# Kernel optimization log

Measured on AMD Instinct MI355X. Metric: run time of the kernel, lower is better.

## Reference

```python
import jax, jax.numpy as jnp
import numpy as np

N_EMBED = 1024
N_HEAD = 16
BLOCK_SIZE = 2048
ROPE_BASE = 10000.0


def _rope_cache():
    # theta uses n_embed (full model dim) as denominator, as in the source,
    # then is truncated to head_size//2 frequencies.
    hs_half = N_EMBED // N_HEAD // 2
    j = jnp.arange(N_EMBED // 2, dtype=jnp.float32)
    theta = jnp.power(ROPE_BASE, -2.0 * j / N_EMBED)
    seq_idx = jnp.arange(BLOCK_SIZE, dtype=jnp.float32)
    idx_theta = jnp.einsum('i,j->ij', seq_idx, theta)[:, :hs_half]  # [block, hs/2]
    return jnp.stack([jnp.cos(idx_theta), jnp.sin(idx_theta)], axis=-1)  # [block, hs/2, 2]


def _apply_rope(x, cache):
    # x: [B, nh, T, hs]. FAITHFUL to source: rope indexes its cache by dim-1,
    # which here is the HEAD dim (rope is called after transpose(1,2)).
    B, d1, d2, hs = x.shape
    rc = cache[:d1, :hs // 2]            # [d1, hs/2, 2]
    rc = rc[None, :, None, :, :]          # [1, d1, 1, hs/2, 2]
    x2 = x.reshape(B, d1, d2, hs // 2, 2)
    cos, sin = rc[..., 0], rc[..., 1]
    xr, xi = x2[..., 0], x2[..., 1]
    rot = jnp.stack([xr * cos - xi * sin, xi * cos + xr * sin], axis=-1)
    return rot.reshape(B, d1, d2, hs).astype(x.dtype)


def setup_inputs() -> dict:
    key = jax.random.key(0)
    ks = jax.random.split(key, 5)
    B, T, C = 2, 2048, N_EMBED
    return {
        'x': jax.random.normal(ks[0], (B, T, C), dtype=jnp.float32),
        'w_attn': jax.random.normal(ks[1], (C, 3 * C), dtype=jnp.float32) * 0.02,
        'b_attn': jax.random.normal(ks[2], (3 * C,), dtype=jnp.float32) * 0.02,
        'w_proj': jax.random.normal(ks[3], (C, C), dtype=jnp.float32) * 0.02,
        'b_proj': jax.random.normal(ks[4], (C,), dtype=jnp.float32) * 0.02,
    }


def reference(x, w_attn, b_attn, w_proj, b_proj):
    B, T, C = x.shape
    nh, hs = N_HEAD, C // N_HEAD
    qkv = x @ w_attn + b_attn                     # [B, T, 3C]
    q, k, v = jnp.split(qkv, 3, axis=-1)
    q = q.reshape(B, T, nh, hs).transpose(0, 2, 1, 3)  # [B, nh, T, hs]
    k = k.reshape(B, T, nh, hs).transpose(0, 2, 1, 3)
    v = v.reshape(B, T, nh, hs).transpose(0, 2, 1, 3)
    cache = _rope_cache()
    q = _apply_rope(q, cache)
    k = _apply_rope(k, cache)
    scale = 1.0 / jnp.sqrt(jnp.asarray(hs, dtype=q.dtype))
    scores = jnp.einsum('bhqd,bhkd->bhqk', q, k) * scale
    causal = jnp.tril(jnp.ones((T, T), dtype=bool))
    scores = jnp.where(causal[None, None], scores, jnp.finfo(scores.dtype).min)
    attn = jax.nn.softmax(scores, axis=-1)
    y = jnp.einsum('bhqk,bhkd->bhqd', attn, v)    # [B, nh, T, hs]
    y = y.transpose(0, 2, 1, 3).reshape(B, T, C)
    return y @ w_proj + b_proj
```

## Files before the change

### kernel.cpp

```cpp
#include <hip/hip_runtime.h>
#include <hip/hip_bf16.h>
#include <math.h>

#define TSEQ 2048
#define CEMB 1024
#define NHEAD 16
#define HS 64

typedef __attribute__((ext_vector_type(8))) short bf16x8;
typedef __attribute__((ext_vector_type(4))) float f32x4;
typedef __attribute__((ext_vector_type(16))) float f32x16;
typedef unsigned int u32;
typedef unsigned long long u64;

__device__ __forceinline__ void gload16(const void* g, void* l) {
    __builtin_amdgcn_global_load_lds(
        (const __attribute__((address_space(1))) unsigned int*)g,
        (__attribute__((address_space(3))) unsigned int*)l, 16, 0, 0);
}

__device__ __forceinline__ u32 pk2(float a, float b) {
    union { u32 u; __hip_bfloat16 h[2]; } t;
    t.h[0] = __float2bfloat16(a); t.h[1] = __float2bfloat16(b);
    return t.u;
}

__global__ void rope_tbl_k(float* __restrict__ tbl) {
    int i = blockIdx.x * blockDim.x + threadIdx.x;
    if (i >= NHEAD * 32) return;
    int h = i >> 5, j = i & 31;
    double theta = pow(10000.0, -2.0 * (double)j / 1024.0);
    double ang = (double)h * theta;
    tbl[2 * i + 0] = (float)cos(ang);
    tbl[2 * i + 1] = (float)sin(ang);
}

__global__ __launch_bounds__(256) void cvt_bf16_k(const float* __restrict__ in,
                                                  __hip_bfloat16* __restrict__ out) {
    int i = (blockIdx.x * 256 + threadIdx.x) * 8;
    float4 a = *(const float4*)(in + i);
    float4 b = *(const float4*)(in + i + 4);
    union { bf16x8 v; __hip_bfloat16 h[8]; } pk;
    pk.h[0] = __float2bfloat16(a.x); pk.h[1] = __float2bfloat16(a.y);
    pk.h[2] = __float2bfloat16(a.z); pk.h[3] = __float2bfloat16(a.w);
    pk.h[4] = __float2bfloat16(b.x); pk.h[5] = __float2bfloat16(b.y);
    pk.h[6] = __float2bfloat16(b.z); pk.h[7] = __float2bfloat16(b.w);
    *(bf16x8*)(out + i) = pk.v;
}

__global__ __launch_bounds__(256) void transpose_bf16_k(const float* __restrict__ src,
                                                        __hip_bfloat16* __restrict__ dst,
                                                        int K, int N) {
    __shared__ float tile[32][33];
    int n0 = blockIdx.x * 32, k0 = blockIdx.y * 32;
    int tx = threadIdx.x & 31, ty = threadIdx.x >> 5;
#pragma unroll
    for (int i = 0; i < 32; i += 8)
        tile[ty + i][tx] = src[(size_t)(k0 + ty + i) * N + n0 + tx];
    __syncthreads();
#pragma unroll
    for (int i = 0; i < 32; i += 8)
        dst[(size_t)(n0 + ty + i) * K + k0 + tx] = __float2bfloat16(tile[tx][ty + i]);
}

__global__ __launch_bounds__(256) void qkv_mfma_k(
    const __hip_bfloat16* __restrict__ Xb, const __hip_bfloat16* __restrict__ Wt,
    const float* __restrict__ bias, const float* __restrict__ tbl,
    __hip_bfloat16* __restrict__ Qb, __hip_bfloat16* __restrict__ Kb,
    __hip_bfloat16* __restrict__ Vtb)
{
    __shared__ __hip_bfloat16 SM[4][128 * 32];
    const int tid = threadIdx.x;
    const int lane = tid & 63, w = tid >> 6;
    const int lr = lane & 15, lg = lane >> 4;
    const int wm = w >> 1, wn = w & 1;
    const int n0 = blockIdx.x * 128;
    const int m0 = blockIdx.y * 128;
    const __hip_bfloat16* gA = Xb + (size_t)(m0 + (tid >> 2)) * CEMB + (tid & 3) * 8;
    const __hip_bfloat16* gB = Wt + (size_t)(n0 + (tid >> 2)) * CEMB + (tid & 3) * 8;
#define QSTAGE(buf, kk) do { \
        gload16(gA + (kk), &SM[buf][tid * 8]); \
        gload16(gA + 64 * CEMB + (kk), &SM[buf][2048 + tid * 8]); \
        gload16(gB + (kk), &SM[2 + (buf)][tid * 8]); \
        gload16(gB + 64 * CEMB + (kk), &SM[2 + (buf)][2048 + tid * 8]); } while (0)
    f32x4 acc[4][4] = {};
    QSTAGE(0, 0);
    __syncthreads();
    for (int k0 = 0; k0 < CEMB; k0 += 32) {
        const int cur = (k0 >> 5) & 1;
        if (k0 + 32 < CEMB) QSTAGE(cur ^ 1, k0 + 32);
        bf16x8 af[4], bfr[4];
#pragma unroll
        for (int mi = 0; mi < 4; ++mi)
            af[mi] = *(const bf16x8*)&SM[cur][(wm * 64 + mi * 16 + lr) * 32 + lg * 8];
#pragma unroll
        for (int ni = 0; ni < 4; ++ni)
            bfr[ni] = *(const bf16x8*)&SM[2 + cur][(wn * 64 + ni * 16 + lr) * 32 + lg * 8];
#pragma unroll
        for (int mi = 0; mi < 4; ++mi)
#pragma unroll
            for (int ni = 0; ni < 4; ++ni)
                acc[mi][ni] = __builtin_amdgcn_mfma_f32_16x16x32_bf16(af[mi], bfr[ni], acc[mi][ni], 0, 0, 0);
        __syncthreads();
    }
    const int sec = (n0 >> 10);
    const int bb = m0 >> 11;
    const int t0v = m0 & 2047;
    if (sec == 2) {
        char* T = (char*)SM;
#pragma unroll
        for (int mi = 0; mi < 4; ++mi) {
#pragma unroll
            for (int ni = 0; ni < 4; ++ni) {
                const int nl = wn * 64 + ni * 16 + lr;
                const float bv = bias[n0 + nl];
                const int mb = wm * 64 + mi * 16 + lg * 4;
                union { u64 u; __hip_bfloat16 hh[4]; } pk;
#pragma unroll
                for (int r = 0; r < 4; ++r) pk.hh[r] = __float2bfloat16(acc[mi][ni][r] + bv);
                *(u64*)(T + nl * 256 + ((mb * 2) ^ ((nl & 7) << 4))) = pk.u;
            }
        }
        __syncthreads();
        const int h0 = (n0 & 1023) >> 6;
#pragma unroll
        for (int i = 0; i < 8; ++i) {
            int cid = tid + 256 * i;
            int n = cid >> 4, mc = cid & 15;
            bf16x8 v = *(const bf16x8*)(T + n * 256 + ((mc * 16) ^ ((n & 7) << 4)));
            *(bf16x8*)&Vtb[(((size_t)bb * NHEAD + h0 + (n >> 6)) * HS + (n & 63)) * TSEQ + t0v + mc * 8] = v;
        }
    } else {
#pragma unroll
        for (int mi = 0; mi < 4; ++mi) {
#pragma unroll
            for (int ni = 0; ni < 4; ++ni) {
                const int gcol = n0 + wn * 64 + ni * 16 + lr;
                const int c63 = gcol & 63;
                const int h = (gcol & 1023) >> 6;
                const int j = c63 >> 1;
                const float cth = tbl[(h * 32 + j) * 2 + 0];
                const float sth = tbl[(h * 32 + j) * 2 + 1];
                const float bv = bias[gcol];
                const int growb = m0 + wm * 64 + mi * 16 + lg * 4;
                const int t0 = growb & 2047;
                const float sc = (sec == 0) ? 0.18033688011112042f : 1.0f;
                __hip_bfloat16* dst = (sec == 0) ? Qb : Kb;
#pragma unroll
                for (int r = 0; r < 4; ++r) {
                    float val = acc[mi][ni][r] + bv;
                    float prt = __shfl_xor(val, 1);
                    float rot = (lr & 1) ? (val * cth + prt * sth) : (val * cth - prt * sth);
                    dst[(((size_t)bb * NHEAD + h) * TSEQ + t0 + r) * HS + c63] = __float2bfloat16(rot * sc);
                }
            }
        }
    }
#undef QSTAGE
}

__global__ __launch_bounds__(128) void attn_k(
    const __hip_bfloat16* __restrict__ Q, const __hip_bfloat16* __restrict__ K,
    const __hip_bfloat16* __restrict__ Vt, __hip_bfloat16* __restrict__ Y)
{
    __shared__ __hip_bfloat16 KsBuf[2][64 * 64];
    __shared__ __hip_bfloat16 VsBuf[2][64 * 64];
    const int tid = threadIdx.x;
    const int w = tid >> 6;
    const int lane = tid & 63;
    const int l31 = lane & 31;
    const int hi = lane >> 5;
    const int id = blockIdx.x;
    const int bh = id & 31;
    const int g = id >> 5, ga = g & 7, gb = g >> 3;
    const int qb = gb * 8 + ((gb & 1) ? (7 - ga) : ga);
    const size_t bho = (size_t)bh * TSEQ * HS;
    const int qw = qb * 64 + w * 32;

    int srcK[4], srcV[4];
#pragma unroll
    for (int j = 0; j < 4; ++j) {
        int L = (tid + 128 * j) * 16;
        int row = L >> 7;
        int ce = ((L & 127) ^ (((row ^ (row >> 3)) & 7) << 4)) >> 1;
        srcK[j] = row * HS + ce;
        srcV[j] = row * TSEQ + ce;
    }
    const __hip_bfloat16* Kg = K + bho;
    const __hip_bfloat16* Vg = Vt + bho;
#define ASTAGE(buf, kt_) do { \
        const __hip_bfloat16* kg_ = Kg + (size_t)(kt_) * 64 * HS; \
        const __hip_bfloat16* vg_ = Vg + (size_t)(kt_) * 64; \
        char* kb_ = (char*)KsBuf[buf]; char* vb_ = (char*)VsBuf[buf]; \
        _Pragma("unroll") \
        for (int j = 0; j < 4; ++j) { \
            gload16(kg_ + srcK[j], kb_ + (tid + 128 * j) * 16); \
            gload16(vg_ + srcV[j], vb_ + (tid + 128 * j) * 16); } } while (0)

    bf16x8 qf[4];
    {
        const __hip_bfloat16* qp = Q + bho + (size_t)(qw + l31) * HS + hi * 8;
#pragma unroll
        for (int kb = 0; kb < 4; ++kb) qf[kb] = *(const bf16x8*)(qp + kb * 16);
    }
    const int base0 = l31 * 128;
    const int swz0 = ((l31 ^ (l31 >> 3)) & 7) << 4;
    const int r32 = 32 + l31;
    const int base1 = r32 * 128;
    const int swz1 = ((r32 ^ (r32 >> 3)) & 7) << 4;

    float mrow = -1e30f, lsum = 0.f;
    f32x16 o0 = {}, o1 = {};

    ASTAGE(0, 0);
    __syncthreads();
    for (int kt = 0; kt <= qb; ++kt) {
        const int cur = kt & 1;
        if (kt < qb) ASTAGE(cur ^ 1, kt + 1);
        const char* KsB = (const char*)KsBuf[cur];
        const char* VsB = (const char*)VsBuf[cur];
        const bool do1 = (w == 1) || (kt < qb);
        f32x16 s0 = {}, s1 = {};
        __builtin_amdgcn_s_setprio(1);
#pragma unroll
        for (int kb = 0; kb < 4; ++kb) {
            bf16x8 kf = *(const bf16x8*)(KsB + base0 + ((kb * 32 + hi * 16) ^ swz0));
            s0 = __builtin_amdgcn_mfma_f32_32x32x16_bf16(kf, qf[kb], s0, 0, 0, 0);
        }
        if (do1) {
#pragma unroll
            for (int kb = 0; kb < 4; ++kb) {
                bf16x8 kf = *(const bf16x8*)(KsB + base1 + ((kb * 32 + hi * 16) ^ swz1));
                s1 = __builtin_amdgcn_mfma_f32_32x32x16_bf16(kf, qf[kb], s1, 0, 0, 0);
            }
        }
        __builtin_amdgcn_s_setprio(0);
        if (kt == qb) {
            if (w == 0) {
#pragma unroll
                for (int r = 0; r < 16; ++r) {
                    int crow = (r & 3) + 8 * (r >> 2) + 4 * hi;
                    if (crow > l31) s0[r] = -1e30f;
                }
            } else {
#pragma unroll
                for (int r = 0; r < 16; ++r) {
                    int crow = (r & 3) + 8 * (r >> 2) + 4 * hi;
                    if (crow > l31) s1[r] = -1e30f;
                }
            }
        }
        float mx = s0[0];
#pragma unroll
        for (int r = 1; r < 16; ++r) mx = fmaxf(mx, s0[r]);
        if (do1) {
#pragma unroll
            for (int r = 0; r < 16; ++r) mx = fmaxf(mx, s1[r]);
        }
        mx = fmaxf(mx, __shfl_xor(mx, 32));
        const float mn = fmaxf(mrow, mx);
        const float alpha = __builtin_amdgcn_exp2f(mrow - mn);
        mrow = mn;
        float ls = 0.f;
#pragma unroll
        for (int r = 0; r < 16; ++r) { s0[r] = __builtin_amdgcn_exp2f(s0[r] - mn); ls += s0[r]; }
        if (do1) {
#pragma unroll
            for (int r = 0; r < 16; ++r) { s1[r] = __builtin_amdgcn_exp2f(s1[r] - mn); ls += s1[r]; }
        }
        ls += __shfl_xor(ls, 32);
        lsum = lsum * alpha + ls;
        o0 = o0 * alpha;
        o1 = o1 * alpha;
        union { u32 u[4]; bf16x8 v; } pa[4];
        {
            u32 w01 = pk2(s0[0], s0[1]),   w23 = pk2(s0[2], s0[3]);
            u32 w45 = pk2(s0[4], s0[5]),   w67 = pk2(s0[6], s0[7]);
            u32 w89 = pk2(s0[8], s0[9]),   wab = pk2(s0[10], s0[11]);
            u32 wcd = pk2(s0[12], s0[13]), wef = pk2(s0[14], s0[15]);
            u32 xa = __shfl_xor(hi ? w01 : w45, 32);
            u32 xb = __shfl_xor(hi ? w23 : w67, 32);
            u32 xc = __shfl_xor(hi ? w89 : wcd, 32);
            u32 xd = __shfl_xor(hi ? wab : wef, 32);
            if (hi == 0) {
                pa[0].u[0] = w01; pa[0].u[1] = w23; pa[0].u[2] = xa;  pa[0].u[3] = xb;
                pa[1].u[0] = w89; pa[1].u[1] = wab; pa[1].u[2] = xc;  pa[1].u[3] = xd;
            } else {
                pa[0].u[0] = xa;  pa[0].u[1] = xb;  pa[0].u[2] = w45; pa[0].u[3] = w67;
                pa[1].u[0] = xc;  pa[1].u[1] = xd;  pa[1].u[2] = wcd; pa[1].u[3] = wef;
            }
        }
        if (do1) {
            u32 w01 = pk2(s1[0], s1[1]),   w23 = pk2(s1[2], s1[3]);
            u32 w45 = pk2(s1[4], s1[5]),   w67 = pk2(s1[6], s1[7]);
            u32 w89 = pk2(s1[8], s1[9]),   wab = pk2(s1[10], s1[11]);
            u32 wcd = pk2(s1[12], s1[13]), wef = pk2(s1[14], s1[15]);
            u32 xa = __shfl_xor(hi ? w01 : w45, 32);
            u32 xb = __shfl_xor(hi ? w23 : w67, 32);
            u32 xc = __shfl_xor(hi ? w89 : wcd, 32);
            u32 xd = __shfl_xor(hi ? wab : wef, 32);
            if (hi == 0) {
                pa[2].u[0] = w01; pa[2].u[1] = w23; pa[2].u[2] = xa;  pa[2].u[3] = xb;
                pa[3].u[0] = w89; pa[3].u[1] = wab; pa[3].u[2] = xc;  pa[3].u[3] = xd;
            } else {
                pa[2].u[0] = xa;  pa[2].u[1] = xb;  pa[2].u[2] = w45; pa[2].u[3] = w67;
                pa[3].u[0] = xc;  pa[3].u[1] = xd;  pa[3].u[2] = wcd; pa[3].u[3] = wef;
            }
        }
        __builtin_amdgcn_s_setprio(1);
#pragma unroll
        for (int ks = 0; ks < 2; ++ks) {
            bf16x8 vf0 = *(const bf16x8*)(VsB + base0 + ((ks * 32 + hi * 16) ^ swz0));
            o0 = __builtin_amdgcn_mfma_f32_32x32x16_bf16(vf0, pa[ks].v, o0, 0, 0, 0);
            bf16x8 vf1 = *(const bf16x8*)(VsB + base1 + ((ks * 32 + hi * 16) ^ swz1));
            o1 = __builtin_amdgcn_mfma_f32_32x32x16_bf16(vf1, pa[ks].v, o1, 0, 0, 0);
        }
        if (do1) {
#pragma unroll
            for (int ks = 2; ks < 4; ++ks) {
                bf16x8 vf0 = *(const bf16x8*)(VsB + base0 + ((ks * 32 + hi * 16) ^ swz0));
                o0 = __builtin_amdgcn_mfma_f32_32x32x16_bf16(vf0, pa[ks].v, o0, 0, 0, 0);
                bf16x8 vf1 = *(const bf16x8*)(VsB + base1 + ((ks * 32 + hi * 16) ^ swz1));
                o1 = __builtin_amdgcn_mfma_f32_32x32x16_bf16(vf1, pa[ks].v, o1, 0, 0, 0);
            }
        }
        __builtin_amdgcn_s_setprio(0);
        __syncthreads();
    }
    __syncthreads();
    {
        char* T = (char*)KsBuf[0] + w * 4096;
        const float inv = 1.f / lsum;
        const int tsw = (l31 & 7) << 4;
#pragma unroll
        for (int r = 0; r < 16; ++r) {
            int d0 = (r & 3) + 8 * (r >> 2) + 4 * hi;
            *(__hip_bfloat16*)(T + base0 + ((d0 * 2) ^ tsw)) = __float2bfloat16(o0[r] * inv);
            *(__hip_bfloat16*)(T + base0 + (((d0 + 32) * 2) ^ tsw)) = __float2bfloat16(o1[r] * inv);
        }
        const int b = bh >> 4, h = bh & 15;
#pragma unroll
        for (int p = 0; p < 4; ++p) {
            int q = p * 8 + (lane >> 3);
            int colb = ((lane & 7) * 16) ^ ((q & 7) << 4);
            bf16x8 v = *(const bf16x8*)(T + q * 128 + colb);
            *(bf16x8*)(Y + ((size_t)b * TSEQ + qw + q) * CEMB + h * HS + (lane & 7) * 8) = v;
        }
    }
#undef ASTAGE
}

__global__ __launch_bounds__(256) void proj_mfma_k(
    const __hip_bfloat16* __restrict__ Ab, const __hip_bfloat16* __restrict__ Wt,
    const float* __restrict__ bias, float* __restrict__ out)
{
    __shared__ __hip_bfloat16 Al[2][128 * 32];
    __shared__ __hip_bfloat16 Bl[2][128 * 32];
    const int tid = threadIdx.x;
    const int lane = tid & 63, w = tid >> 6;
    const int lr = lane & 15, lg = lane >> 4;
    const int wm = w >> 1, wn = w & 1;
    const int n0 = blockIdx.x * 128;
    const int m0 = blockIdx.y * 128;
    const __hip_bfloat16* gA = Ab + (size_t)(m0 + (tid >> 2)) * CEMB + (tid & 3) * 8;
    const __hip_bfloat16* gB = Wt + (size_t)(n0 + (tid >> 2)) * CEMB + (tid & 3) * 8;
#define PSTAGE(buf, kk) do { \
        gload16(gA + (kk), &Al[buf][tid * 8]); \
        gload16(gA + 64 * CEMB + (kk), &Al[buf][2048 + tid * 8]); \
        gload16(gB + (kk), &Bl[buf][tid * 8]); \
        gload16(gB + 64 * CEMB + (kk), &Bl[buf][2048 + tid * 8]); } while (0)
    f32x4 acc[4][4] = {};
    PSTAGE(0, 0);
    __syncthreads();
    for (int k0 = 0; k0 < CEMB; k0 += 32) {
        const int cur = (k0 >> 5) & 1;
        if (k0 + 32 < CEMB) PSTAGE(cur ^ 1, k0 + 32);
        bf16x8 af[4], bfr[4];
#pragma unroll
        for (int mi = 0; mi < 4; ++mi)
            af[mi] = *(const bf16x8*)&Al[cur][(wm * 64 + mi * 16 + lr) * 32 + lg * 8];
#pragma unroll
        for (int ni = 0; ni < 4; ++ni)
            bfr[ni] = *(const bf16x8*)&Bl[cur][(wn * 64 + ni * 16 + lr) * 32 + lg * 8];
#pragma unroll
        for (int mi = 0; mi < 4; ++mi)
#pragma unroll
            for (int ni = 0; ni < 4; ++ni)
                acc[mi][ni] = __builtin_amdgcn_mfma_f32_16x16x32_bf16(af[mi], bfr[ni], acc[mi][ni], 0, 0, 0);
        __syncthreads();
    }
#pragma unroll
    for (int mi = 0; mi < 4; ++mi) {
#pragma unroll
        for (int ni = 0; ni < 4; ++ni) {
            const int gcol = n0 + wn * 64 + ni * 16 + lr;
            const float bv = bias[gcol];
            const int growb = m0 + wm * 64 + mi * 16 + lg * 4;
#pragma unroll
            for (int r = 0; r < 4; ++r)
                out[(size_t)(growb + r) * CEMB + gcol] = acc[mi][ni][r] + bv;
        }
    }
#undef PSTAGE
}

extern "C" void kernel_launch(void* const* d_in, const int* in_sizes, int n_in,
                              void* d_out, int out_size, void* d_ws, size_t ws_size,
                              hipStream_t stream)
{
    const float* x      = (const float*)d_in[0];
    const float* w_attn = (const float*)d_in[1];
    const float* b_attn = (const float*)d_in[2];
    const float* w_proj = (const float*)d_in[3];
    const float* b_proj = (const float*)d_in[4];
    float* out = (float*)d_out;
    char* base = (char*)d_ws;

    const size_t MB = 1048576;
    float* tbl          = (float*)base;
    __hip_bfloat16* Xb  = (__hip_bfloat16*)(base + 4096);
    __hip_bfloat16* Wta = (__hip_bfloat16*)(base + 4096 + 8 * MB);
    __hip_bfloat16* Wpt = (__hip_bfloat16*)(base + 4096 + 14 * MB);
    __hip_bfloat16* Qb  = (__hip_bfloat16*)(base + 4096 + 16 * MB);
    __hip_bfloat16* Kb  = (__hip_bfloat16*)(base + 4096 + 24 * MB);
    __hip_bfloat16* Vtb = (__hip_bfloat16*)(base + 4096 + 32 * MB);
    __hip_bfloat16* Yb  = Xb;

    rope_tbl_k<<<1, 512, 0, stream>>>(tbl);
    cvt_bf16_k<<<2048, 256, 0, stream>>>(x, Xb);
    transpose_bf16_k<<<dim3(96, 32), 256, 0, stream>>>(w_attn, Wta, CEMB, 3 * CEMB);
    transpose_bf16_k<<<dim3(32, 32), 256, 0, stream>>>(w_proj, Wpt, CEMB, CEMB);
    qkv_mfma_k<<<dim3(24, 32), 256, 0, stream>>>(Xb, Wta, b_attn, tbl, Qb, Kb, Vtb);
    attn_k<<<1024, 128, 0, stream>>>(Qb, Kb, Vtb, Yb);
    proj_mfma_k<<<dim3(8, 32), 256, 0, stream>>>(Yb, Wpt, b_proj, out);
}
```

Baseline: 147.6 us.

## Process 128-key tiles per iteration with single-buffered K/V instead of double buffering

The attention loop now consumes 128 keys per iteration (four 32-row score blocks) instead of 64, halving the number of iterations, softmax rescales and barriers. K/V staging goes from a double-buffered prefetch overlapped with compute to a single buffer loaded after each iteration's barrier, with a new V swizzle for the 256-byte rows. This trades away load/compute overlap and adds register pressure (four score accumulators, eight P fragments) in exchange for fewer loop overheads and more MFMA work per sync.

```diff
diff --git a/kernel.cpp b/kernel.cpp
--- a/kernel.cpp
+++ b/kernel.cpp
@@ -163,8 +163,8 @@
     const __hip_bfloat16* __restrict__ Q, const __hip_bfloat16* __restrict__ K,
     const __hip_bfloat16* __restrict__ Vt, __hip_bfloat16* __restrict__ Y)
 {
-    __shared__ __hip_bfloat16 KsBuf[2][64 * 64];
-    __shared__ __hip_bfloat16 VsBuf[2][64 * 64];
+    __shared__ __hip_bfloat16 Ks[128 * 64];
+    __shared__ __hip_bfloat16 Vs[64 * 128];
     const int tid = threadIdx.x;
     const int w = tid >> 6;
     const int lane = tid & 63;
@@ -177,23 +177,23 @@
     const size_t bho = (size_t)bh * TSEQ * HS;
     const int qw = qb * 64 + w * 32;
 
-    int srcK[4], srcV[4];
-#pragma unroll
-    for (int j = 0; j < 4; ++j) {
+    int srcK[8], srcV[8];
+#pragma unroll
+    for (int j = 0; j < 8; ++j) {
         int L = (tid + 128 * j) * 16;
-        int row = L >> 7;
-        int ce = ((L & 127) ^ (((row ^ (row >> 3)) & 7) << 4)) >> 1;
-        srcK[j] = row * HS + ce;
-        srcV[j] = row * TSEQ + ce;
+        int rk = L >> 7;
+        srcK[j] = rk * HS + (((L & 127) ^ (((rk ^ (rk >> 3)) & 7) << 4)) >> 1);
+        int rv = L >> 8;
+        srcV[j] = rv * TSEQ + (((L & 255) ^ ((rv & 15) << 4)) >> 1);
     }
     const __hip_bfloat16* Kg = K + bho;
     const __hip_bfloat16* Vg = Vt + bho;
-#define ASTAGE(buf, kt_) do { \
-        const __hip_bfloat16* kg_ = Kg + (size_t)(kt_) * 64 * HS; \
-        const __hip_bfloat16* vg_ = Vg + (size_t)(kt_) * 64; \
-        char* kb_ = (char*)KsBuf[buf]; char* vb_ = (char*)VsBuf[buf]; \
+#define ASTAGE(r_) do { \
+        const __hip_bfloat16* kg_ = Kg + (size_t)(r_) * 128 * HS; \
+        const __hip_bfloat16* vg_ = Vg + (size_t)(r_) * 128; \
+        char* kb_ = (char*)Ks; char* vb_ = (char*)Vs; \
         _Pragma("unroll") \
-        for (int j = 0; j < 4; ++j) { \
+        for (int j = 0; j < 8; ++j) { \
             gload16(kg_ + srcK[j], kb_ + (tid + 128 * j) * 16); \
             gload16(vg_ + srcV[j], vb_ + (tid + 128 * j) * 16); } } while (0)
 
@@ -203,59 +203,100 @@
 #pragma unroll
         for (int kb = 0; kb < 4; ++kb) qf[kb] = *(const bf16x8*)(qp + kb * 16);
     }
-    const int base0 = l31 * 128;
-    const int swz0 = ((l31 ^ (l31 >> 3)) & 7) << 4;
-    const int r32 = 32 + l31;
-    const int base1 = r32 * 128;
-    const int swz1 = ((r32 ^ (r32 >> 3)) & 7) << 4;
+    int kbase[4], kswz[4];
+#pragma unroll
+    for (int st = 0; st < 4; ++st) {
+        int row = st * 32 + l31;
+        kbase[st] = row * 128;
+        kswz[st] = ((row ^ (row >> 3)) & 7) << 4;
+    }
+    const int vswz = (l31 & 15) << 4;
+    const int vbase0 = l31 * 256;
+    const int vbase1 = (32 + l31) * 256;
 
     float mrow = -1e30f, lsum = 0.f;
     f32x16 o0 = {}, o1 = {};
 
-    ASTAGE(0, 0);
+    const int nr = (qb >> 1) + 1;
+    const int diag = 2 * (qb & 1) + w;
+
+    ASTAGE(0);
     __syncthreads();
-    for (int kt = 0; kt <= qb; ++kt) {
-        const int cur = kt & 1;
-        if (kt < qb) ASTAGE(cur ^ 1, kt + 1);
-        const char* KsB = (const char*)KsBuf[cur];
-        const char* VsB = (const char*)VsBuf[cur];
-        const bool do1 = (w == 1) || (kt < qb);
-        f32x16 s0 = {}, s1 = {};
+    for (int r = 0; r < nr; ++r) {
+        const bool last = (r == nr - 1);
+        const bool a1 = !last || (diag >= 1);
+        const bool a2 = !last || (diag >= 2);
+        const bool a3 = !last || (diag >= 3);
+        f32x16 s0 = {}, s1 = {}, s2 = {}, s3 = {};
         __builtin_amdgcn_s_setprio(1);
 #pragma unroll
         for (int kb = 0; kb < 4; ++kb) {
-            bf16x8 kf = *(const bf16x8*)(KsB + base0 + ((kb * 32 + hi * 16) ^ swz0));
+            bf16x8 kf = *(const bf16x8*)((const char*)Ks + kbase[0] + ((kb * 32 + hi * 16) ^ kswz[0]));
             s0 = __builtin_amdgcn_mfma_f32_32x32x16_bf16(kf, qf[kb], s0, 0, 0, 0);
         }
-        if (do1) {
+        if (a1) {
 #pragma unroll
             for (int kb = 0; kb < 4; ++kb) {
-                bf16x8 kf = *(const bf16x8*)(KsB + base1 + ((kb * 32 + hi * 16) ^ swz1));
+                bf16x8 kf = *(const bf16x8*)((const char*)Ks + kbase[1] + ((kb * 32 + hi * 16) ^ kswz[1]));
                 s1 = __builtin_amdgcn_mfma_f32_32x32x16_bf16(kf, qf[kb], s1, 0, 0, 0);
             }
         }
+        if (a2) {
+#pragma unroll
+            for (int kb = 0; kb < 4; ++kb) {
+                bf16x8 kf = *(const bf16x8*)((const char*)Ks + kbase[2] + ((kb * 32 + hi * 16) ^ kswz[2]));
+                s2 = __builtin_amdgcn_mfma_f32_32x32x16_bf16(kf, qf[kb], s2, 0, 0, 0);
+            }
+        }
+        if (a3) {
+#pragma unroll
+            for (int kb = 0; kb < 4; ++kb) {
+                bf16x8 kf = *(const bf16x8*)((const char*)Ks + kbase[3] + ((kb * 32 + hi * 16) ^ kswz[3]));
+                s3 = __builtin_amdgcn_mfma_f32_32x32x16_bf16(kf, qf[kb], s3, 0, 0, 0);
+            }
+        }
         __builtin_amdgcn_s_setprio(0);
-        if (kt == qb) {
-            if (w == 0) {
-#pragma unroll
-                for (int r = 0; r < 16; ++r) {
-                    int crow = (r & 3) + 8 * (r >> 2) + 4 * hi;
-                    if (crow > l31) s0[r] = -1e30f;
+        if (last) {
+            if (diag == 0) {
+#pragma unroll
+                for (int rr = 0; rr < 16; ++rr) {
+                    int crow = (rr & 3) + 8 * (rr >> 2) + 4 * hi;
+                    if (crow > l31) s0[rr] = -1e30f;
+                }
+            } else if (diag == 1) {
+#pragma unroll
+                for (int rr = 0; rr < 16; ++rr) {
+                    int crow = (rr & 3) + 8 * (rr >> 2) + 4 * hi;
+                    if (crow > l31) s1[rr] = -1e30f;
+                }
+            } else if (diag == 2) {
+#pragma unroll
+                for (int rr = 0; rr < 16; ++rr) {
+                    int crow = (rr & 3) + 8 * (rr >> 2) + 4 * hi;
+                    if (crow > l31) s2[rr] = -1e30f;
                 }
             } else {
 #pragma unroll
-                for (int r = 0; r < 16; ++r) {
-                    int crow = (r & 3) + 8 * (r >> 2) + 4 * hi;
-                    if (crow > l31) s1[r] = -1e30f;
+                for (int rr = 0; rr < 16; ++rr) {
+                    int crow = (rr & 3) + 8 * (rr >> 2) + 4 * hi;
+                    if (crow > l31) s3[rr] = -1e30f;
                 }
             }
         }
         float mx = s0[0];
 #pragma unroll
-        for (int r = 1; r < 16; ++r) mx = fmaxf(mx, s0[r]);
-        if (do1) {
-#pragma unroll
-            for (int r = 0; r < 16; ++r) mx = fmaxf(mx, s1[r]);
+        for (int rr = 1; rr < 16; ++rr) mx = fmaxf(mx, s0[rr]);
+        if (a1) {
+#pragma unroll
+            for (int rr = 0; rr < 16; ++rr) mx = fmaxf(mx, s1[rr]);
+        }
+        if (a2) {
+#pragma unroll
+            for (int rr = 0; rr < 16; ++rr) mx = fmaxf(mx, s2[rr]);
+        }
+        if (a3) {
+#pragma unroll
+            for (int rr = 0; rr < 16; ++rr) mx = fmaxf(mx, s3[rr]);
         }
         mx = fmaxf(mx, __shfl_xor(mx, 32));
         const float mn = fmaxf(mrow, mx);
@@ -263,80 +304,73 @@
         mrow = mn;
         float ls = 0.f;
 #pragma unroll
-        for (int r = 0; r < 16; ++r) { s0[r] = __builtin_amdgcn_exp2f(s0[r] - mn); ls += s0[r]; }
-        if (do1) {
-#pragma unroll
-            for (int r = 0; r < 16; ++r) { s1[r] = __builtin_amdgcn_exp2f(s1[r] - mn); ls += s1[r]; }
+        for (int rr = 0; rr < 16; ++rr) { s0[rr] = __builtin_amdgcn_exp2f(s0[rr] - mn); ls += s0[rr]; }
+        if (a1) {
+#pragma unroll
+            for (int rr = 0; rr < 16; ++rr) { s1[rr] = __builtin_amdgcn_exp2f(s1[rr] - mn); ls += s1[rr]; }
+        }
+        if (a2) {
+#pragma unroll
+            for (int rr = 0; rr < 16; ++rr) { s2[rr] = __builtin_amdgcn_exp2f(s2[rr] - mn); ls += s2[rr]; }
+        }
+        if (a3) {
+#pragma unroll
+            for (int rr = 0; rr < 16; ++rr) { s3[rr] = __builtin_amdgcn_exp2f(s3[rr] - mn); ls += s3[rr]; }
         }
         ls += __shfl_xor(ls, 32);
         lsum = lsum * alpha + ls;
         o0 = o0 * alpha;
         o1 = o1 * alpha;
-        union { u32 u[4]; bf16x8 v; } pa[4];
-        {
-            u32 w01 = pk2(s0[0], s0[1]),   w23 = pk2(s0[2], s0[3]);
-            u32 w45 = pk2(s0[4], s0[5]),   w67 = pk2(s0[6], s0[7]);
-            u32 w89 = pk2(s0[8], s0[9]),   wab = pk2(s0[10], s0[11]);
-            u32 wcd = pk2(s0[12], s0[13]), wef = pk2(s0[14], s0[15]);
-            u32 xa = __shfl_xor(hi ? w01 : w45, 32);
-            u32 xb = __shfl_xor(hi ? w23 : w67, 32);
-            u32 xc = __shfl_xor(hi ? w89 : wcd, 32);
-            u32 xd = __shfl_xor(hi ? wab : wef, 32);
-            if (hi == 0) {
-                pa[0].u[0] = w01; pa[0].u[1] = w23; pa[0].u[2] = xa;  pa[0].u[3] = xb;
-                pa[1].u[0] = w89; pa[1].u[1] = wab; pa[1].u[2] = xc;  pa[1].u[3] = xd;
-            } else {
-                pa[0].u[0] = xa;  pa[0].u[1] = xb;  pa[0].u[2] = w45; pa[0].u[3] = w67;
-                pa[1].u[0] = xc;  pa[1].u[1] = xd;  pa[1].u[2] = wcd; pa[1].u[3] = wef;
-            }
-        }
-        if (do1) {
-            u32 w01 = pk2(s1[0], s1[1]),   w23 = pk2(s1[2], s1[3]);
-            u32 w45 = pk2(s1[4], s1[5]),   w67 = pk2(s1[6], s1[7]);
-            u32 w89 = pk2(s1[8], s1[9]),   wab = pk2(s1[10], s1[11]);
-            u32 wcd = pk2(s1[12], s1[13]), wef = pk2(s1[14], s1[15]);
-            u32 xa = __shfl_xor(hi ? w01 : w45, 32);
-            u32 xb = __shfl_xor(hi ? w23 : w67, 32);
-            u32 xc = __shfl_xor(hi ? w89 : wcd, 32);
-            u32 xd = __shfl_xor(hi ? wab : wef, 32);
-            if (hi == 0) {
-                pa[2].u[0] = w01; pa[2].u[1] = w23; pa[2].u[2] = xa;  pa[2].u[3] = xb;
-                pa[3].u[0] = w89; pa[3].u[1] = wab; pa[3].u[2] = xc;  pa[3].u[3] = xd;
-            } else {
-                pa[2].u[0] = xa;  pa[2].u[1] = xb;  pa[2].u[2] = w45; pa[2].u[3] = w67;
-                pa[3].u[0] = xc;  pa[3].u[1] = xd;  pa[3].u[2] = wcd; pa[3].u[3] = wef;
-            }
-        }
+        union { u32 u[4]; bf16x8 v; } pa[8];
+#define PACK(S, P0, P1) do { \
+            u32 w01 = pk2(S[0], S[1]),   w23 = pk2(S[2], S[3]); \
+            u32 w45 = pk2(S[4], S[5]),   w67 = pk2(S[6], S[7]); \
+            u32 w89 = pk2(S[8], S[9]),   wab = pk2(S[10], S[11]); \
+            u32 wcd = pk2(S[12], S[13]), wef = pk2(S[14], S[15]); \
+            u32 xa = __shfl_xor(hi ? w01 : w45, 32); \
+            u32 xb = __shfl_xor(hi ? w23 : w67, 32); \
+            u32 xc = __shfl_xor(hi ? w89 : wcd, 32); \
+            u32 xd = __shfl_xor(hi ? wab : wef, 32); \
+            if (hi == 0) { \
+                pa[P0].u[0] = w01; pa[P0].u[1] = w23; pa[P0].u[2] = xa;  pa[P0].u[3] = xb; \
+                pa[P1].u[0] = w89; pa[P1].u[1] = wab; pa[P1].u[2] = xc;  pa[P1].u[3] = xd; \
+            } else { \
+                pa[P0].u[0] = xa;  pa[P0].u[1] = xb;  pa[P0].u[2] = w45; pa[P0].u[3] = w67; \
+                pa[P1].u[0] = xc;  pa[P1].u[1] = xd;  pa[P1].u[2] = wcd; pa[P1].u[3] = wef; \
+            } } while (0)
+        PACK(s0, 0, 1);
+        if (a1) PACK(s1, 2, 3);
+        if (a2) PACK(s2, 4, 5);
+        if (a3) PACK(s3, 6, 7);
+#undef PACK
         __builtin_amdgcn_s_setprio(1);
-#pragma unroll
-        for (int ks = 0; ks < 2; ++ks) {
-            bf16x8 vf0 = *(const bf16x8*)(VsB + base0 + ((ks * 32 + hi * 16) ^ swz0));
-            o0 = __builtin_amdgcn_mfma_f32_32x32x16_bf16(vf0, pa[ks].v, o0, 0, 0, 0);
-            bf16x8 vf1 = *(const bf16x8*)(VsB + base1 + ((ks * 32 + hi * 16) ^ swz1));
-            o1 = __builtin_amdgcn_mfma_f32_32x32x16_bf16(vf1, pa[ks].v, o1, 0, 0, 0);
-        }
-        if (do1) {
-#pragma unroll
-            for (int ks = 2; ks < 4; ++ks) {
-                bf16x8 vf0 = *(const bf16x8*)(VsB + base0 + ((ks * 32 + hi * 16) ^ swz0));
-                o0 = __builtin_amdgcn_mfma_f32_32x32x16_bf16(vf0, pa[ks].v, o0, 0, 0, 0);
-                bf16x8 vf1 = *(const bf16x8*)(VsB + base1 + ((ks * 32 + hi * 16) ^ swz1));
-                o1 = __builtin_amdgcn_mfma_f32_32x32x16_bf16(vf1, pa[ks].v, o1, 0, 0, 0);
-            }
-        }
+#define PVC(ks) do { \
+            bf16x8 vf0 = *(const bf16x8*)((const char*)Vs + vbase0 + (((ks) * 32 + hi * 16) ^ vswz)); \
+            o0 = __builtin_amdgcn_mfma_f32_32x32x16_bf16(vf0, pa[ks].v, o0, 0, 0, 0); \
+            bf16x8 vf1 = *(const bf16x8*)((const char*)Vs + vbase1 + (((ks) * 32 + hi * 16) ^ vswz)); \
+            o1 = __builtin_amdgcn_mfma_f32_32x32x16_bf16(vf1, pa[ks].v, o1, 0, 0, 0); } while (0)
+        PVC(0); PVC(1);
+        if (a1) { PVC(2); PVC(3); }
+        if (a2) { PVC(4); PVC(5); }
+        if (a3) { PVC(6); PVC(7); }
+#undef PVC
         __builtin_amdgcn_s_setprio(0);
         __syncthreads();
-    }
-    __syncthreads();
+        if (r + 1 < nr) {
+            ASTAGE(r + 1);
+            __syncthreads();
+        }
+    }
     {
-        char* T = (char*)KsBuf[0] + w * 4096;
+        char* T = (char*)Ks + w * 4096;
         const float inv = 1.f / lsum;
         const int tsw = (l31 & 7) << 4;
-#pragma unroll
-        for (int r = 0; r < 16; ++r) {
-            int d0 = (r & 3) + 8 * (r >> 2) + 4 * hi;
-            *(__hip_bfloat16*)(T + base0 + ((d0 * 2) ^ tsw)) = __float2bfloat16(o0[r] * inv);
-            *(__hip_bfloat16*)(T + base0 + (((d0 + 32) * 2) ^ tsw)) = __float2bfloat16(o1[r] * inv);
+        const int tbase = l31 * 128;
+#pragma unroll
+        for (int rr = 0; rr < 16; ++rr) {
+            int d0 = (rr & 3) + 8 * (rr >> 2) + 4 * hi;
+            *(__hip_bfloat16*)(T + tbase + ((d0 * 2) ^ tsw)) = __float2bfloat16(o0[rr] * inv);
+            *(__hip_bfloat16*)(T + tbase + (((d0 + 32) * 2) ^ tsw)) = __float2bfloat16(o1[rr] * inv);
         }
         const int b = bh >> 4, h = bh & 15;
 #pragma unroll
```

After: 151.5 us. 1.03x slower.

## Split long causal attention rows across two blocks and merge partial softmax

Applied to the files above, without the earlier changes.

Replaces the 128-thread per-64-query attention kernel with a 256-thread kernel over 128-query tiles. The long tiles (query blocks 8-15) are split into two KV halves whose partial outputs, maxima and sums are written to workspace in fp32. A new merge kernel then combines them into bf16 Y, with a static unit table ordering blocks for load balance. The aim is to remove the tail imbalance of causal attention at the cost of an extra launch, fp32 partial traffic, and a fallback to the old kernel when the workspace is too small.

```diff
diff --git a/kernel.cpp b/kernel.cpp
--- a/kernel.cpp
+++ b/kernel.cpp
@@ -24,6 +24,10 @@
     t.h[0] = __float2bfloat16(a); t.h[1] = __float2bfloat16(b);
     return t.u;
 }
+
+__device__ const int UNIT_TBL[24] = {22,7,20,21,19,17,6,14,
+                                     23,18,16,12,4,5,13,15,
+                                     0,1,2,3,10,8,9,11};
 
 __global__ void rope_tbl_k(float* __restrict__ tbl) {
     int i = blockIdx.x * blockDim.x + threadIdx.x;
@@ -159,7 +163,245 @@
 #undef QSTAGE
 }
 
-__global__ __launch_bounds__(128) void attn_k(
+__global__ __launch_bounds__(256) void attn_split_k(
+    const __hip_bfloat16* __restrict__ Q, const __hip_bfloat16* __restrict__ K,
+    const __hip_bfloat16* __restrict__ Vt, __hip_bfloat16* __restrict__ Y,
+    float* __restrict__ Op, float* __restrict__ Mp, float* __restrict__ Lp)
+{
+    __shared__ __hip_bfloat16 KsBuf[2][64 * 64];
+    __shared__ __hip_bfloat16 VsBuf[2][64 * 64];
+    const int tid = threadIdx.x;
+    const int w = tid >> 6;
+    const int lane = tid & 63;
+    const int l31 = lane & 31;
+    const int hi = lane >> 5;
+    const int id = blockIdx.x;
+    const int bh = id & 31;
+    const int u = UNIT_TBL[id >> 5];
+    int qbb, kt0, ktN, half;
+    bool split;
+    if (u < 8) { qbb = u; half = 0; kt0 = 0; ktN = 2 * u + 2; split = false; }
+    else {
+        qbb = 8 + ((u - 8) >> 1); half = (u - 8) & 1;
+        kt0 = half ? (qbb + 1) : 0;
+        ktN = half ? (2 * qbb + 2) : (qbb + 1);
+        split = true;
+    }
+    const size_t bho = (size_t)bh * TSEQ * HS;
+    const int Qw = qbb * 128 + w * 32;
+
+    int srcK[2], srcV[2];
+#pragma unroll
+    for (int j = 0; j < 2; ++j) {
+        int L = (tid + 256 * j) * 16;
+        int row = L >> 7;
+        int ce = ((L & 127) ^ (((row ^ (row >> 3)) & 7) << 4)) >> 1;
+        srcK[j] = row * HS + ce;
+        srcV[j] = row * TSEQ + ce;
+    }
+    const __hip_bfloat16* Kg = K + bho;
+    const __hip_bfloat16* Vg = Vt + bho;
+#define ASTAGE(buf, kt_) do { \
+        const __hip_bfloat16* kg_ = Kg + (size_t)(kt_) * 64 * HS; \
+        const __hip_bfloat16* vg_ = Vg + (size_t)(kt_) * 64; \
+        char* kb_ = (char*)KsBuf[buf]; char* vb_ = (char*)VsBuf[buf]; \
+        _Pragma("unroll") \
+        for (int j = 0; j < 2; ++j) { \
+            gload16(kg_ + srcK[j], kb_ + (tid + 256 * j) * 16); \
+            gload16(vg_ + srcV[j], vb_ + (tid + 256 * j) * 16); } } while (0)
+
+    bf16x8 qf[4];
+    {
+        const __hip_bfloat16* qp = Q + bho + (size_t)(Qw + l31) * HS + hi * 8;
+#pragma unroll
+        for (int kb = 0; kb < 4; ++kb) qf[kb] = *(const bf16x8*)(qp + kb * 16);
+    }
+    const int base0 = l31 * 128;
+    const int swz0 = ((l31 ^ (l31 >> 3)) & 7) << 4;
+    const int r32 = 32 + l31;
+    const int base1 = r32 * 128;
+    const int swz1 = ((r32 ^ (r32 >> 3)) & 7) << 4;
+
+    float mrow = -1e30f, lsum = 0.f;
+    f32x16 o0 = {}, o1 = {};
+
+    ASTAGE(0, kt0);
+    __syncthreads();
+    for (int kt = kt0; kt < ktN; ++kt) {
+        const int cur = (kt - kt0) & 1;
+        if (kt + 1 < ktN) ASTAGE(cur ^ 1, kt + 1);
+        const char* KsB = (const char*)KsBuf[cur];
+        const char* VsB = (const char*)VsBuf[cur];
+        const int kvb0 = kt * 64, kvb1 = kt * 64 + 32;
+        const bool do0 = kvb0 <= Qw;
+        const bool do1 = kvb1 <= Qw;
+        if (do0) {
+            f32x16 s0 = {}, s1 = {};
+            __builtin_amdgcn_s_setprio(1);
+#pragma unroll
+            for (int kb = 0; kb < 4; ++kb) {
+                bf16x8 kf = *(const bf16x8*)(KsB + base0 + ((kb * 32 + hi * 16) ^ swz0));
+                s0 = __builtin_amdgcn_mfma_f32_32x32x16_bf16(kf, qf[kb], s0, 0, 0, 0);
+            }
+            if (do1) {
+#pragma unroll
+                for (int kb = 0; kb < 4; ++kb) {
+                    bf16x8 kf = *(const bf16x8*)(KsB + base1 + ((kb * 32 + hi * 16) ^ swz1));
+                    s1 = __builtin_amdgcn_mfma_f32_32x32x16_bf16(kf, qf[kb], s1, 0, 0, 0);
+                }
+            }
+            __builtin_amdgcn_s_setprio(0);
+            if (kvb0 == Qw) {
+#pragma unroll
+                for (int r = 0; r < 16; ++r) {
+                    int crow = (r & 3) + 8 * (r >> 2) + 4 * hi;
+                    if (crow > l31) s0[r] = -1e30f;
+                }
+            }
+            if (do1 && kvb1 == Qw) {
+#pragma unroll
+                for (int r = 0; r < 16; ++r) {
+                    int crow = (r & 3) + 8 * (r >> 2) + 4 * hi;
+                    if (crow > l31) s1[r] = -1e30f;
+                }
+            }
+            float mx = s0[0];
+#pragma unroll
+            for (int r = 1; r < 16; ++r) mx = fmaxf(mx, s0[r]);
+            if (do1) {
+#pragma unroll
+                for (int r = 0; r < 16; ++r) mx = fmaxf(mx, s1[r]);
+            }
+            mx = fmaxf(mx, __shfl_xor(mx, 32));
+            const float mn = fmaxf(mrow, mx);
+            const float alpha = __builtin_amdgcn_exp2f(mrow - mn);
+            mrow = mn;
+            float ls = 0.f;
+#pragma unroll
+            for (int r = 0; r < 16; ++r) { s0[r] = __builtin_amdgcn_exp2f(s0[r] - mn); ls += s0[r]; }
+            if (do1) {
+#pragma unroll
+                for (int r = 0; r < 16; ++r) { s1[r] = __builtin_amdgcn_exp2f(s1[r] - mn); ls += s1[r]; }
+            }
+            ls += __shfl_xor(ls, 32);
+            lsum = lsum * alpha + ls;
+            o0 = o0 * alpha;
+            o1 = o1 * alpha;
+            union { u32 u[4]; bf16x8 v; } pa[4];
+            {
+                u32 w01 = pk2(s0[0], s0[1]),   w23 = pk2(s0[2], s0[3]);
+                u32 w45 = pk2(s0[4], s0[5]),   w67 = pk2(s0[6], s0[7]);
+                u32 w89 = pk2(s0[8], s0[9]),   wab = pk2(s0[10], s0[11]);
+                u32 wcd = pk2(s0[12], s0[13]), wef = pk2(s0[14], s0[15]);
+                u32 xa = __shfl_xor(hi ? w01 : w45, 32);
+                u32 xb = __shfl_xor(hi ? w23 : w67, 32);
+                u32 xc = __shfl_xor(hi ? w89 : wcd, 32);
+                u32 xd = __shfl_xor(hi ? wab : wef, 32);
+                if (hi == 0) {
+                    pa[0].u[0] = w01; pa[0].u[1] = w23; pa[0].u[2] = xa;  pa[0].u[3] = xb;
+                    pa[1].u[0] = w89; pa[1].u[1] = wab; pa[1].u[2] = xc;  pa[1].u[3] = xd;
+                } else {
+                    pa[0].u[0] = xa;  pa[0].u[1] = xb;  pa[0].u[2] = w45; pa[0].u[3] = w67;
+                    pa[1].u[0] = xc;  pa[1].u[1] = xd;  pa[1].u[2] = wcd; pa[1].u[3] = wef;
+                }
+            }
+            if (do1) {
+                u32 w01 = pk2(s1[0], s1[1]),   w23 = pk2(s1[2], s1[3]);
+                u32 w45 = pk2(s1[4], s1[5]),   w67 = pk2(s1[6], s1[7]);
+                u32 w89 = pk2(s1[8], s1[9]),   wab = pk2(s1[10], s1[11]);
+                u32 wcd = pk2(s1[12], s1[13]), wef = pk2(s1[14], s1[15]);
+                u32 xa = __shfl_xor(hi ? w01 : w45, 32);
+                u32 xb = __shfl_xor(hi ? w23 : w67, 32);
+                u32 xc = __shfl_xor(hi ? w89 : wcd, 32);
+                u32 xd = __shfl_xor(hi ? wab : wef, 32);
+                if (hi == 0) {
+                    pa[2].u[0] = w01; pa[2].u[1] = w23; pa[2].u[2] = xa;  pa[2].u[3] = xb;
+                    pa[3].u[0] = w89; pa[3].u[1] = wab; pa[3].u[2] = xc;  pa[3].u[3] = xd;
+                } else {
+                    pa[2].u[0] = xa;  pa[2].u[1] = xb;  pa[2].u[2] = w45; pa[2].u[3] = w67;
+                    pa[3].u[0] = xc;  pa[3].u[1] = xd;  pa[3].u[2] = wcd; pa[3].u[3] = wef;
+                }
+            }
+            __builtin_amdgcn_s_setprio(1);
+#define PVC(ks) do { \
+                bf16x8 vf0 = *(const bf16x8*)(VsB + base0 + (((ks) * 32 + hi * 16) ^ swz0)); \
+                o0 = __builtin_amdgcn_mfma_f32_32x32x16_bf16(vf0, pa[ks].v, o0, 0, 0, 0); \
+                bf16x8 vf1 = *(const bf16x8*)(VsB + base1 + (((ks) * 32 + hi * 16) ^ swz1)); \
+                o1 = __builtin_amdgcn_mfma_f32_32x32x16_bf16(vf1, pa[ks].v, o1, 0, 0, 0); } while (0)
+            PVC(0); PVC(1);
+            if (do1) { PVC(2); PVC(3); }
+#undef PVC
+            __builtin_amdgcn_s_setprio(0);
+        }
+        __syncthreads();
+    }
+    if (!split) {
+        char* T = (char*)KsBuf + w * 4096;
+        const float inv = 1.f / lsum;
+        const int tsw = (l31 & 7) << 4;
+        const int tbase = l31 * 128;
+#pragma unroll
+        for (int r = 0; r < 16; ++r) {
+            int d0 = (r & 3) + 8 * (r >> 2) + 4 * hi;
+            *(__hip_bfloat16*)(T + tbase + ((d0 * 2) ^ tsw)) = __float2bfloat16(o0[r] * inv);
+            *(__hip_bfloat16*)(T + tbase + (((d0 + 32) * 2) ^ tsw)) = __float2bfloat16(o1[r] * inv);
+        }
+        const int b = bh >> 4, h = bh & 15;
+#pragma unroll
+        for (int p = 0; p < 4; ++p) {
+            int q = p * 8 + (lane >> 3);
+            int colb = ((lane & 7) * 16) ^ ((q & 7) << 4);
+            bf16x8 v = *(const bf16x8*)(T + q * 128 + colb);
+            *(bf16x8*)(Y + ((size_t)b * TSEQ + Qw + q) * CEMB + h * HS + (lane & 7) * 8) = v;
+        }
+    } else {
+        const int p = bh * 16 + (qbb - 8) * 2 + half;
+        float* Ob = Op + (size_t)p * 8192;
+        const int qloc = w * 32 + l31;
+#pragma unroll
+        for (int r = 0; r < 16; ++r) {
+            int d0 = (r & 3) + 8 * (r >> 2) + 4 * hi;
+            Ob[d0 * 128 + qloc] = o0[r];
+            Ob[(d0 + 32) * 128 + qloc] = o1[r];
+        }
+        if (hi == 0) {
+            Mp[p * 128 + qloc] = mrow;
+            Lp[p * 128 + qloc] = lsum;
+        }
+    }
+#undef ASTAGE
+}
+
+__global__ __launch_bounds__(256) void merge_k(
+    const float* __restrict__ Op, const float* __restrict__ Mp,
+    const float* __restrict__ Lp, __hip_bfloat16* __restrict__ Y)
+{
+    const int blk = blockIdx.x;
+    const int bh = blk & 31, qq = blk >> 5;
+    const int p0 = bh * 16 + qq * 2, p1 = p0 + 1;
+    const int t = threadIdx.x;
+    const int q = t >> 1, dg = (t & 1) * 32;
+    const float m0 = Mp[p0 * 128 + q], m1 = Mp[p1 * 128 + q];
+    const float l0 = Lp[p0 * 128 + q], l1 = Lp[p1 * 128 + q];
+    const float m = fmaxf(m0, m1);
+    const float w0 = exp2f(m0 - m), w1 = exp2f(m1 - m);
+    const float inv = 1.f / (l0 * w0 + l1 * w1);
+    const float* O0 = Op + (size_t)p0 * 8192;
+    const float* O1 = Op + (size_t)p1 * 8192;
+    union { bf16x8 v[4]; __hip_bfloat16 h[32]; } outp;
+#pragma unroll
+    for (int i = 0; i < 32; ++i) {
+        int d = dg + i;
+        outp.h[i] = __float2bfloat16((O0[d * 128 + q] * w0 + O1[d * 128 + q] * w1) * inv);
+    }
+    const int b = bh >> 4, h = bh & 15;
+    const int qg = (8 + qq) * 128 + q;
+    __hip_bfloat16* yp = Y + ((size_t)b * TSEQ + qg) * CEMB + h * HS + dg;
+#pragma unroll
+    for (int i = 0; i < 4; ++i) *(bf16x8*)(yp + i * 8) = outp.v[i];
+}
+
+__global__ __launch_bounds__(128) void attn_full_k(
     const __hip_bfloat16* __restrict__ Q, const __hip_bfloat16* __restrict__ K,
     const __hip_bfloat16* __restrict__ Vt, __hip_bfloat16* __restrict__ Y)
 {
@@ -176,7 +418,6 @@
     const int qb = gb * 8 + ((gb & 1) ? (7 - ga) : ga);
     const size_t bho = (size_t)bh * TSEQ * HS;
     const int qw = qb * 64 + w * 32;
-
     int srcK[4], srcV[4];
 #pragma unroll
     for (int j = 0; j < 4; ++j) {
@@ -196,7 +437,6 @@
         for (int j = 0; j < 4; ++j) { \
             gload16(kg_ + srcK[j], kb_ + (tid + 128 * j) * 16); \
             gload16(vg_ + srcV[j], vb_ + (tid + 128 * j) * 16); } } while (0)
-
     bf16x8 qf[4];
     {
         const __hip_bfloat16* qp = Q + bho + (size_t)(qw + l31) * HS + hi * 8;
@@ -208,10 +448,8 @@
     const int r32 = 32 + l31;
     const int base1 = r32 * 128;
     const int swz1 = ((r32 ^ (r32 >> 3)) & 7) << 4;
-
     float mrow = -1e30f, lsum = 0.f;
     f32x16 o0 = {}, o1 = {};
-
     ASTAGE(0, 0);
     __syncthreads();
     for (int kt = 0; kt <= qb; ++kt) {
@@ -308,26 +546,17 @@
             }
         }
         __builtin_amdgcn_s_setprio(1);
-#pragma unroll
-        for (int ks = 0; ks < 2; ++ks) {
-            bf16x8 vf0 = *(const bf16x8*)(VsB + base0 + ((ks * 32 + hi * 16) ^ swz0));
-            o0 = __builtin_amdgcn_mfma_f32_32x32x16_bf16(vf0, pa[ks].v, o0, 0, 0, 0);
-            bf16x8 vf1 = *(const bf16x8*)(VsB + base1 + ((ks * 32 + hi * 16) ^ swz1));
-            o1 = __builtin_amdgcn_mfma_f32_32x32x16_bf16(vf1, pa[ks].v, o1, 0, 0, 0);
-        }
-        if (do1) {
-#pragma unroll
-            for (int ks = 2; ks < 4; ++ks) {
-                bf16x8 vf0 = *(const bf16x8*)(VsB + base0 + ((ks * 32 + hi * 16) ^ swz0));
-                o0 = __builtin_amdgcn_mfma_f32_32x32x16_bf16(vf0, pa[ks].v, o0, 0, 0, 0);
-                bf16x8 vf1 = *(const bf16x8*)(VsB + base1 + ((ks * 32 + hi * 16) ^ swz1));
-                o1 = __builtin_amdgcn_mfma_f32_32x32x16_bf16(vf1, pa[ks].v, o1, 0, 0, 0);
-            }
-        }
+#define PVC(ks) do { \
+            bf16x8 vf0 = *(const bf16x8*)(VsB + base0 + (((ks) * 32 + hi * 16) ^ swz0)); \
+            o0 = __builtin_amdgcn_mfma_f32_32x32x16_bf16(vf0, pa[ks].v, o0, 0, 0, 0); \
+            bf16x8 vf1 = *(const bf16x8*)(VsB + base1 + (((ks) * 32 + hi * 16) ^ swz1)); \
+            o1 = __builtin_amdgcn_mfma_f32_32x32x16_bf16(vf1, pa[ks].v, o1, 0, 0, 0); } while (0)
+        PVC(0); PVC(1);
+        if (do1) { PVC(2); PVC(3); }
+#undef PVC
         __builtin_amdgcn_s_setprio(0);
         __syncthreads();
     }
-    __syncthreads();
     {
         char* T = (char*)KsBuf[0] + w * 4096;
         const float inv = 1.f / lsum;
@@ -425,12 +654,22 @@
     __hip_bfloat16* Kb  = (__hip_bfloat16*)(base + 4096 + 24 * MB);
     __hip_bfloat16* Vtb = (__hip_bfloat16*)(base + 4096 + 32 * MB);
     __hip_bfloat16* Yb  = Xb;
+    const size_t PART_OFF = 4096 + 40 * MB;
+    float* Op = (float*)(base + PART_OFF);
+    float* Mp = Op + (size_t)512 * 8192;
+    float* Lp = Mp + (size_t)512 * 128;
+    const size_t need = PART_OFF + 16 * MB + 512 * 1024;
 
     rope_tbl_k<<<1, 512, 0, stream>>>(tbl);
     cvt_bf16_k<<<2048, 256, 0, stream>>>(x, Xb);
     transpose_bf16_k<<<dim3(96, 32), 256, 0, stream>>>(w_attn, Wta, CEMB, 3 * CEMB);
     transpose_bf16_k<<<dim3(32, 32), 256, 0, stream>>>(w_proj, Wpt, CEMB, CEMB);
     qkv_mfma_k<<<dim3(24, 32), 256, 0, stream>>>(Xb, Wta, b_attn, tbl, Qb, Kb, Vtb);
-    attn_k<<<1024, 128, 0, stream>>>(Qb, Kb, Vtb, Yb);
+    if (ws_size >= need) {
+        attn_split_k<<<768, 256, 0, stream>>>(Qb, Kb, Vtb, Yb, Op, Mp, Lp);
+        merge_k<<<256, 256, 0, stream>>>(Op, Mp, Lp, Yb);
+    } else {
+        attn_full_k<<<1024, 128, 0, stream>>>(Qb, Kb, Vtb, Yb);
+    }
     proj_mfma_k<<<dim3(8, 32), 256, 0, stream>>>(Yb, Wpt, b_proj, out);
 }
```

Result: faster. 129.2 us (-12.5%).
